# Optimization experiments

Hardware: AMD Instinct MI355X
Metric: run time of the kernel (lower is better)

## Reference

```python
import jax, jax.numpy as jnp
import numpy as np

S, D_IN, H = 8192, 1024, 2048  # seq_len, input dim (vector_sizes[level]), hidden (vector_sizes[level+1])


def setup_inputs() -> dict:
    key = jax.random.key(0)
    k1, k2, k3 = jax.random.split(key, 3)
    inputs = jax.random.normal(k1, (S, D_IN), dtype=jnp.float32)
    W = jax.random.normal(k2, (D_IN, 4 * H), dtype=jnp.float32) * 0.02  # input kernel
    U = jax.random.normal(k3, (H, 4 * H), dtype=jnp.float32) * 0.02    # recurrent kernel
    b = jnp.zeros((4 * H,), dtype=jnp.float32)                          # bias
    return {"inputs": inputs, "W": W, "U": U, "b": b}


def reference(inputs, W, U, b):
    # Keras LSTMCell with activation='linear' (cell/output activation = identity),
    # recurrent_activation = sigmoid, gate order i, f, c, o.
    # RNN(return_sequences=False) -> return last hidden state only.
    h0 = jnp.zeros((H,), dtype=inputs.dtype)
    c0 = jnp.zeros((H,), dtype=inputs.dtype)
    # Precompute input projections for all timesteps: [S, 4H]
    xz = inputs @ W + b

    def step(carry, xz_t):
        h, c = carry
        z = xz_t + h @ U                      # [4H]
        zi, zf, zg, zo = jnp.split(z, 4)
        i = jax.nn.sigmoid(zi)
        f = jax.nn.sigmoid(zf)
        o = jax.nn.sigmoid(zo)
        c_new = f * c + i * zg                # linear candidate activation
        h_new = o * c_new                     # linear output activation
        return (h_new, c_new), None

    (h_last, _), _ = jax.lax.scan(step, (h0, c0), xz)
    return h_last
```

## Files before the change

### kernel.cpp

```cpp
#include <hip/hip_runtime.h>
#include <stdint.h>


#define S_LEN   8192
#define D_INP   1024
#define HDIM    2048
#define FH      8192
#define NWG     256
#define TPB     256
#define XB      8
#define PACE_MAX 120

typedef _Float16 half2_t __attribute__((ext_vector_type(2)));

#if defined(__has_builtin)
#if __has_builtin(__builtin_amdgcn_fdot2)
#define HAVE_FDOT2 1
#endif
#endif

__device__ __forceinline__ float fdot2f(uint32_t a, uint32_t b, float c) {
#ifdef HAVE_FDOT2
    return __builtin_amdgcn_fdot2(__builtin_bit_cast(half2_t, a),
                                  __builtin_bit_cast(half2_t, b), c, false);
#else
    half2_t ha = __builtin_bit_cast(half2_t, a);
    half2_t hb = __builtin_bit_cast(half2_t, b);
    c = fmaf((float)ha.x, (float)hb.x, c);
    c = fmaf((float)ha.y, (float)hb.y, c);
    return c;
#endif
}

__device__ __forceinline__ uint32_t pack2(float a, float b) {
    half2_t h;
    h.x = (_Float16)a;
    h.y = (_Float16)b;
    return __builtin_bit_cast(uint32_t, h);
}

__device__ __forceinline__ float sigmoidf_fast(float z) {
    return 1.0f / (1.0f + __expf(-z));
}

__device__ __forceinline__ unsigned long long ald(const unsigned long long* p) {
    return __hip_atomic_load(p, __ATOMIC_RELAXED, __HIP_MEMORY_SCOPE_AGENT);
}

extern "C" __global__ void __launch_bounds__(TPB, 1)
lstm_persist(const float* __restrict__ x, const float* __restrict__ W,
             const float* __restrict__ U, const float* __restrict__ b,
             float* __restrict__ out, unsigned long long* __restrict__ hbuf)
{
    __shared__ __align__(16) uint32_t xl[XB * 640];
    __shared__ __align__(16) float    zz[2][4 * 8 * 4];

    const int tid  = threadIdx.x;
    const int wg   = blockIdx.x;
    const int cg   = tid & 7;
    const int kc   = tid >> 3;
    const int w    = tid >> 6;
    const int lane = tid & 63;
    const int gb   = lane & 56;

    uint32_t ureg[4][32];
    uint32_t wreg[4][16];
#pragma unroll
    for (int g = 0; g < 4; ++g) {
        const int col = g * HDIM + wg * 8 + cg;
#pragma unroll
        for (int p = 0; p < 32; ++p) {
            const int k0 = kc * 64 + 2 * p;
            ureg[g][p] = pack2(U[(size_t)k0 * FH + col],
                               U[(size_t)(k0 + 1) * FH + col]);
        }
#pragma unroll
        for (int p = 0; p < 16; ++p) {
            const int k0 = kc * 32 + 2 * p;
            wreg[g][p] = pack2(W[(size_t)k0 * FH + col],
                               W[(size_t)(k0 + 1) * FH + col]);
        }
    }
    float bias[4] = {0.f, 0.f, 0.f, 0.f};
    if (tid < 8) {
#pragma unroll
        for (int g = 0; g < 4; ++g) bias[g] = b[g * HDIM + wg * 8 + cg];
    }
    float cst = 0.0f;

    const int xr  = tid >> 5;
    const int kcw = tid & 31;
    float4 pf[8];
    {
        const float4* src = (const float4*)(x + (size_t)xr * D_INP + kcw * 32);
#pragma unroll
        for (int q = 0; q < 8; ++q) pf[q] = src[q];
    }

    unsigned long long* const hb0 = hbuf;
    unsigned long long* const hb1 = hbuf + 1024;

    int pace = 0;

    for (int t = 0; t < S_LEN; ++t) {
        const int s = t & (XB - 1);

        unsigned long long* const gsrc = ((t & 1) ? hb1 : hb0) + tid * 4;
        unsigned long long a0, a1, a2, a3;
        if (t > 0) {
            for (int i = 0; i < pace; ++i) __builtin_amdgcn_s_sleep(1);
            a0 = ald(gsrc + 0); a1 = ald(gsrc + 1);
            a2 = ald(gsrc + 2); a3 = ald(gsrc + 3);
        }

        if (s == 0) {
            uint32_t* dst = &xl[xr * 640 + kcw * 20];
#pragma unroll
            for (int q = 0; q < 4; ++q) {
                uint4 v;
                v.x = pack2(pf[2 * q].x, pf[2 * q].y);
                v.y = pack2(pf[2 * q].z, pf[2 * q].w);
                v.z = pack2(pf[2 * q + 1].x, pf[2 * q + 1].y);
                v.w = pack2(pf[2 * q + 1].z, pf[2 * q + 1].w);
                *(uint4*)(dst + q * 4) = v;
            }
            __syncthreads();
            if (t + XB < S_LEN) {
                const float4* src = (const float4*)(
                    x + (size_t)(t + XB + xr) * D_INP + kcw * 32);
#pragma unroll
                for (int q = 0; q < 8; ++q) pf[q] = src[q];
            }
        }

        float acc[4] = {0.f, 0.f, 0.f, 0.f};
        {
            uint32_t xp[16];
            const uint32_t* xpp = &xl[s * 640 + kc * 20];
            *(uint4*)&xp[0]  = *(const uint4*)(xpp + 0);
            *(uint4*)&xp[4]  = *(const uint4*)(xpp + 4);
            *(uint4*)&xp[8]  = *(const uint4*)(xpp + 8);
            *(uint4*)&xp[12] = *(const uint4*)(xpp + 12);
#pragma unroll
            for (int p = 0; p < 16; ++p) {
#pragma unroll
                for (int g = 0; g < 4; ++g)
                    acc[g] = fdot2f(wreg[g][p], xp[p], acc[g]);
            }
        }

        uint4 q4 = {0u, 0u, 0u, 0u};
        if (t > 0) {
            const unsigned int want = (unsigned int)t;
            bool hit = ((unsigned int)(a0 >> 32) == want) &
                       ((unsigned int)(a1 >> 32) == want) &
                       ((unsigned int)(a2 >> 32) == want) &
                       ((unsigned int)(a3 >> 32) == want);
            if (__all(hit)) {
                if (pace > 0) pace -= 1;
            } else {
                pace = (pace + 8 > PACE_MAX) ? PACE_MAX : pace + 8;
                a0 = ald(gsrc + 0); a1 = ald(gsrc + 1);
                a2 = ald(gsrc + 2); a3 = ald(gsrc + 3);
                hit = ((unsigned int)(a0 >> 32) == want) &
                      ((unsigned int)(a1 >> 32) == want) &
                      ((unsigned int)(a2 >> 32) == want) &
                      ((unsigned int)(a3 >> 32) == want);
                if (!__all(hit)) {
                    int guard = 0;
                    for (;;) {
                        a0 = ald(gsrc + 0); a1 = ald(gsrc + 1);
                        a2 = ald(gsrc + 2); a3 = ald(gsrc + 3);
                        const bool ok = ((unsigned int)(a0 >> 32) == want) &
                                        ((unsigned int)(a1 >> 32) == want) &
                                        ((unsigned int)(a2 >> 32) == want) &
                                        ((unsigned int)(a3 >> 32) == want);
                        if (ok || ++guard >= (1 << 20)) break;
                        __builtin_amdgcn_s_sleep(1);
                    }
                }
            }
            q4.x = (unsigned int)a0;
            q4.y = (unsigned int)a1;
            q4.z = (unsigned int)a2;
            q4.w = (unsigned int)a3;
        }

#pragma unroll
        for (int j = 0; j < 8; ++j) {
            const int sl = gb + j;
            const uint32_t w0 = __shfl(q4.x, sl);
            const uint32_t w1 = __shfl(q4.y, sl);
            const uint32_t w2 = __shfl(q4.z, sl);
            const uint32_t w3 = __shfl(q4.w, sl);
#pragma unroll
            for (int g = 0; g < 4; ++g) {
                acc[g] = fdot2f(ureg[g][4 * j + 0], w0, acc[g]);
                acc[g] = fdot2f(ureg[g][4 * j + 1], w1, acc[g]);
                acc[g] = fdot2f(ureg[g][4 * j + 2], w2, acc[g]);
                acc[g] = fdot2f(ureg[g][4 * j + 3], w3, acc[g]);
            }
        }

#pragma unroll
        for (int g = 0; g < 4; ++g) {
            acc[g] += __shfl_xor(acc[g], 8);
            acc[g] += __shfl_xor(acc[g], 16);
            acc[g] += __shfl_xor(acc[g], 32);
        }
        if (lane < 8) {
            float4 vv = {acc[0], acc[1], acc[2], acc[3]};
            *(float4*)&zz[t & 1][(w * 8 + cg) * 4] = vv;
        }
        __syncthreads();

        if (tid < 8) {
            const float* zp = zz[t & 1];
            const float4 z0 = *(const float4*)&zp[(0 + cg) * 4];
            const float4 z1 = *(const float4*)&zp[(8 + cg) * 4];
            const float4 z2 = *(const float4*)&zp[(16 + cg) * 4];
            const float4 z3 = *(const float4*)&zp[(24 + cg) * 4];
            const float zi = bias[0] + z0.x + z1.x + z2.x + z3.x;
            const float zf = bias[1] + z0.y + z1.y + z2.y + z3.y;
            const float zg = bias[2] + z0.z + z1.z + z2.z + z3.z;
            const float zo = bias[3] + z0.w + z1.w + z2.w + z3.w;
            const float si = sigmoidf_fast(zi);
            const float sf = sigmoidf_fast(zf);
            const float so = sigmoidf_fast(zo);
            const float cn = sf * cst + si * zg;
            cst = cn;
            const float hn = so * cn;
            if (t < S_LEN - 1) {
                const float ha  = __shfl(hn, 2 * cg);
                const float hbv = __shfl(hn, 2 * cg + 1);
                if (cg < 4) {
                    const unsigned long long pv =
                        ((unsigned long long)(unsigned int)(t + 1) << 32) |
                        (unsigned long long)pack2(ha, hbv);
                    unsigned long long* const dst =
                        (((t + 1) & 1) ? hb1 : hb0) + wg * 4 + cg;
                    __hip_atomic_store(dst, pv, __ATOMIC_RELAXED,
                                       __HIP_MEMORY_SCOPE_AGENT);
                }
            } else {
                out[wg * 8 + cg] = hn;
            }
        }
    }
}

extern "C" void kernel_launch(void* const* d_in, const int* in_sizes, int n_in,
                              void* d_out, int out_size, void* d_ws, size_t ws_size,
                              hipStream_t stream) {
    const float* x = (const float*)d_in[0];
    const float* W = (const float*)d_in[1];
    const float* U = (const float*)d_in[2];
    const float* b = (const float*)d_in[3];
    unsigned long long* hbuf = (unsigned long long*)d_ws;

    (void)hipMemsetAsync(hbuf, 0, (size_t)2 * 1024 * sizeof(unsigned long long),
                         stream);

    hipLaunchKernelGGL(lstm_persist, dim3(NWG), dim3(TPB), 0, stream,
                       x, W, U, b, (float*)d_out, hbuf);
}
```

Baseline: 18.48 ms.

## Replace per-step workgroup barrier with LDS flags and double-buffer x staging

The per-timestep __syncthreads is replaced by workgroup-scope release/acquire flags in LDS. Waves 1-3 publish their partial gate sums and wave 0 spins until all three are ready, then reduces and runs the cell update. The x-tile staging moves to a two-buffer LDS scheme filled mid-block, which removes the barrier at block boundaries. The hidden-state loads are also issued before the x staging and pace sleep, so their latency overlaps other work. The aim is to cut barrier and latency stalls on the serial critical path. The cost is spin-waiting in wave 0 and ordering that depends on loose inter-wave lockstep.

```diff
diff --git a/kernel.cpp b/kernel.cpp
--- a/kernel.cpp
+++ b/kernel.cpp
@@ -8,7 +8,6 @@
 #define FH      8192
 #define NWG     256
 #define TPB     256
-#define XB      8
 #define PACE_MAX 120
 
 typedef _Float16 half2_t __attribute__((ext_vector_type(2)));
@@ -52,8 +51,9 @@
              const float* __restrict__ U, const float* __restrict__ b,
              float* __restrict__ out, unsigned long long* __restrict__ hbuf)
 {
-    __shared__ __align__(16) uint32_t xl[XB * 640];
-    __shared__ __align__(16) float    zz[2][4 * 8 * 4];
+    __shared__ __align__(16) uint32_t xl[2][8 * 640];
+    __shared__ __align__(16) float    zz[2][3 * 8 * 4];
+    __shared__ int wflag[3];
 
     const int tid  = threadIdx.x;
     const int wg   = blockIdx.x;
@@ -95,7 +95,23 @@
         const float4* src = (const float4*)(x + (size_t)xr * D_INP + kcw * 32);
 #pragma unroll
         for (int q = 0; q < 8; ++q) pf[q] = src[q];
+        uint32_t* dst = &xl[0][xr * 640 + kcw * 20];
+#pragma unroll
+        for (int q = 0; q < 4; ++q) {
+            uint4 v;
+            v.x = pack2(pf[2 * q].x, pf[2 * q].y);
+            v.y = pack2(pf[2 * q].z, pf[2 * q].w);
+            v.z = pack2(pf[2 * q + 1].x, pf[2 * q + 1].y);
+            v.w = pack2(pf[2 * q + 1].z, pf[2 * q + 1].w);
+            *(uint4*)(dst + q * 4) = v;
+        }
+        const float4* src2 = (const float4*)(x + (size_t)(8 + xr) * D_INP +
+                                             kcw * 32);
+#pragma unroll
+        for (int q = 0; q < 8; ++q) pf[q] = src2[q];
     }
+    if (tid == 0) { wflag[0] = -1; wflag[1] = -1; wflag[2] = -1; }
+    __syncthreads();
 
     unsigned long long* const hb0 = hbuf;
     unsigned long long* const hb1 = hbuf + 1024;
@@ -103,18 +119,18 @@
     int pace = 0;
 
     for (int t = 0; t < S_LEN; ++t) {
-        const int s = t & (XB - 1);
+        const int s = t & 7;
 
         unsigned long long* const gsrc = ((t & 1) ? hb1 : hb0) + tid * 4;
-        unsigned long long a0, a1, a2, a3;
+        unsigned long long p0, p1, p2, p3;
         if (t > 0) {
-            for (int i = 0; i < pace; ++i) __builtin_amdgcn_s_sleep(1);
-            a0 = ald(gsrc + 0); a1 = ald(gsrc + 1);
-            a2 = ald(gsrc + 2); a3 = ald(gsrc + 3);
-        }
-
-        if (s == 0) {
-            uint32_t* dst = &xl[xr * 640 + kcw * 20];
+            p0 = ald(gsrc + 0); p1 = ald(gsrc + 1);
+            p2 = ald(gsrc + 2); p3 = ald(gsrc + 3);
+        }
+
+        if (s == 4 && t + 4 < S_LEN) {
+            const int nb = ((t >> 3) + 1) & 1;
+            uint32_t* dst = &xl[nb][xr * 640 + kcw * 20];
 #pragma unroll
             for (int q = 0; q < 4; ++q) {
                 uint4 v;
@@ -124,19 +140,34 @@
                 v.w = pack2(pf[2 * q + 1].z, pf[2 * q + 1].w);
                 *(uint4*)(dst + q * 4) = v;
             }
-            __syncthreads();
-            if (t + XB < S_LEN) {
+            if (t + 12 < S_LEN) {
                 const float4* src = (const float4*)(
-                    x + (size_t)(t + XB + xr) * D_INP + kcw * 32);
+                    x + (size_t)(t + 12 + xr) * D_INP + kcw * 32);
 #pragma unroll
                 for (int q = 0; q < 8; ++q) pf[q] = src[q];
             }
+        }
+
+        bool phit = false;
+        if (t > 0) {
+            for (int i = 0; i < pace; ++i) __builtin_amdgcn_s_sleep(1);
+            const unsigned int want = (unsigned int)t;
+            const bool ph = ((unsigned int)(p0 >> 32) == want) &
+                            ((unsigned int)(p1 >> 32) == want) &
+                            ((unsigned int)(p2 >> 32) == want) &
+                            ((unsigned int)(p3 >> 32) == want);
+            phit = __all(ph);
+        }
+        unsigned long long a0, a1, a2, a3;
+        if (t > 0 && !phit) {
+            a0 = ald(gsrc + 0); a1 = ald(gsrc + 1);
+            a2 = ald(gsrc + 2); a3 = ald(gsrc + 3);
         }
 
         float acc[4] = {0.f, 0.f, 0.f, 0.f};
         {
             uint32_t xp[16];
-            const uint32_t* xpp = &xl[s * 640 + kc * 20];
+            const uint32_t* xpp = &xl[(t >> 3) & 1][s * 640 + kc * 20];
             *(uint4*)&xp[0]  = *(const uint4*)(xpp + 0);
             *(uint4*)&xp[4]  = *(const uint4*)(xpp + 4);
             *(uint4*)&xp[8]  = *(const uint4*)(xpp + 8);
@@ -152,21 +183,19 @@
         uint4 q4 = {0u, 0u, 0u, 0u};
         if (t > 0) {
             const unsigned int want = (unsigned int)t;
-            bool hit = ((unsigned int)(a0 >> 32) == want) &
-                       ((unsigned int)(a1 >> 32) == want) &
-                       ((unsigned int)(a2 >> 32) == want) &
-                       ((unsigned int)(a3 >> 32) == want);
-            if (__all(hit)) {
-                if (pace > 0) pace -= 1;
+            if (phit) {
+                pace = (pace > 1) ? pace - 2 : 0;
+                q4.x = (unsigned int)p0; q4.y = (unsigned int)p1;
+                q4.z = (unsigned int)p2; q4.w = (unsigned int)p3;
             } else {
-                pace = (pace + 8 > PACE_MAX) ? PACE_MAX : pace + 8;
-                a0 = ald(gsrc + 0); a1 = ald(gsrc + 1);
-                a2 = ald(gsrc + 2); a3 = ald(gsrc + 3);
-                hit = ((unsigned int)(a0 >> 32) == want) &
-                      ((unsigned int)(a1 >> 32) == want) &
-                      ((unsigned int)(a2 >> 32) == want) &
-                      ((unsigned int)(a3 >> 32) == want);
-                if (!__all(hit)) {
+                bool hit = ((unsigned int)(a0 >> 32) == want) &
+                           ((unsigned int)(a1 >> 32) == want) &
+                           ((unsigned int)(a2 >> 32) == want) &
+                           ((unsigned int)(a3 >> 32) == want);
+                if (__all(hit)) {
+                    if (pace > 0) pace -= 1;
+                } else {
+                    pace = (pace + 8 > PACE_MAX) ? PACE_MAX : pace + 8;
                     int guard = 0;
                     for (;;) {
                         a0 = ald(gsrc + 0); a1 = ald(gsrc + 1);
@@ -179,11 +208,9 @@
                         __builtin_amdgcn_s_sleep(1);
                     }
                 }
-            }
-            q4.x = (unsigned int)a0;
-            q4.y = (unsigned int)a1;
-            q4.z = (unsigned int)a2;
-            q4.w = (unsigned int)a3;
+                q4.x = (unsigned int)a0; q4.y = (unsigned int)a1;
+                q4.z = (unsigned int)a2; q4.w = (unsigned int)a3;
+            }
         }
 
 #pragma unroll
@@ -208,42 +235,57 @@
             acc[g] += __shfl_xor(acc[g], 16);
             acc[g] += __shfl_xor(acc[g], 32);
         }
-        if (lane < 8) {
-            float4 vv = {acc[0], acc[1], acc[2], acc[3]};
-            *(float4*)&zz[t & 1][(w * 8 + cg) * 4] = vv;
-        }
-        __syncthreads();
-
-        if (tid < 8) {
-            const float* zp = zz[t & 1];
-            const float4 z0 = *(const float4*)&zp[(0 + cg) * 4];
-            const float4 z1 = *(const float4*)&zp[(8 + cg) * 4];
-            const float4 z2 = *(const float4*)&zp[(16 + cg) * 4];
-            const float4 z3 = *(const float4*)&zp[(24 + cg) * 4];
-            const float zi = bias[0] + z0.x + z1.x + z2.x + z3.x;
-            const float zf = bias[1] + z0.y + z1.y + z2.y + z3.y;
-            const float zg = bias[2] + z0.z + z1.z + z2.z + z3.z;
-            const float zo = bias[3] + z0.w + z1.w + z2.w + z3.w;
-            const float si = sigmoidf_fast(zi);
-            const float sf = sigmoidf_fast(zf);
-            const float so = sigmoidf_fast(zo);
-            const float cn = sf * cst + si * zg;
-            cst = cn;
-            const float hn = so * cn;
-            if (t < S_LEN - 1) {
-                const float ha  = __shfl(hn, 2 * cg);
-                const float hbv = __shfl(hn, 2 * cg + 1);
-                if (cg < 4) {
-                    const unsigned long long pv =
-                        ((unsigned long long)(unsigned int)(t + 1) << 32) |
-                        (unsigned long long)pack2(ha, hbv);
-                    unsigned long long* const dst =
-                        (((t + 1) & 1) ? hb1 : hb0) + wg * 4 + cg;
-                    __hip_atomic_store(dst, pv, __ATOMIC_RELAXED,
-                                       __HIP_MEMORY_SCOPE_AGENT);
+
+        if (w != 0) {
+            if (lane < 8) {
+                float4 vv = {acc[0], acc[1], acc[2], acc[3]};
+                *(float4*)&zz[t & 1][((w - 1) * 8 + cg) * 4] = vv;
+            }
+            if (lane == 0)
+                __hip_atomic_store(&wflag[w - 1], t, __ATOMIC_RELEASE,
+                                   __HIP_MEMORY_SCOPE_WORKGROUP);
+        } else {
+            int guard = 0;
+            for (;;) {
+                const int f0 = __hip_atomic_load(&wflag[0], __ATOMIC_ACQUIRE,
+                                                 __HIP_MEMORY_SCOPE_WORKGROUP);
+                const int f1 = __hip_atomic_load(&wflag[1], __ATOMIC_ACQUIRE,
+                                                 __HIP_MEMORY_SCOPE_WORKGROUP);
+                const int f2 = __hip_atomic_load(&wflag[2], __ATOMIC_ACQUIRE,
+                                                 __HIP_MEMORY_SCOPE_WORKGROUP);
+                if ((f0 >= t) & (f1 >= t) & (f2 >= t)) break;
+                if (++guard >= (1 << 20)) break;
+            }
+            if (lane < 8) {
+                const float* zp = zz[t & 1];
+                const float4 z1 = *(const float4*)&zp[(0 + cg) * 4];
+                const float4 z2 = *(const float4*)&zp[(8 + cg) * 4];
+                const float4 z3 = *(const float4*)&zp[(16 + cg) * 4];
+                const float zi = bias[0] + acc[0] + z1.x + z2.x + z3.x;
+                const float zf = bias[1] + acc[1] + z1.y + z2.y + z3.y;
+                const float zg = bias[2] + acc[2] + z1.z + z2.z + z3.z;
+                const float zo = bias[3] + acc[3] + z1.w + z2.w + z3.w;
+                const float si = sigmoidf_fast(zi);
+                const float sf = sigmoidf_fast(zf);
+                const float so = sigmoidf_fast(zo);
+                const float cn = sf * cst + si * zg;
+                cst = cn;
+                const float hn = so * cn;
+                if (t < S_LEN - 1) {
+                    const float ha  = __shfl(hn, 2 * cg);
+                    const float hbv = __shfl(hn, 2 * cg + 1);
+                    if (cg < 4) {
+                        const unsigned long long pv =
+                            ((unsigned long long)(unsigned int)(t + 1) << 32) |
+                            (unsigned long long)pack2(ha, hbv);
+                        unsigned long long* const dst =
+                            (((t + 1) & 1) ? hb1 : hb0) + wg * 4 + cg;
+                        __hip_atomic_store(dst, pv, __ATOMIC_RELAXED,
+                                           __HIP_MEMORY_SCOPE_AGENT);
+                    }
+                } else {
+                    out[wg * 8 + cg] = hn;
                 }
-            } else {
-                out[wg * 8 + cg] = hn;
             }
         }
     }
```

After: 35.11 ms. +90.0%, slower.
